# Kernel tuning notes

Measured on AMD Instinct MI355X. Metric: run time of the kernel, lower is better.

Reference implementation:

```python
import jax, jax.numpy as jnp
import numpy as np

CH = 256
IC = 128  # inter_channels = channels // reduction
TEMP = 0.05


def setup_inputs() -> dict:
    key = jax.random.key(0)
    k1, k2, k3, k4, k5 = jax.random.split(key, 5)
    x = jax.random.normal(k1, (8, CH, 64, 64), dtype=jnp.float32)
    # 1x1 conv weights stored as [out_ch, in_ch]
    w_qkv = jax.random.normal(k2, (3 * IC, CH), dtype=jnp.float32) * 0.01
    b_qkv = jax.random.normal(k3, (3 * IC,), dtype=jnp.float32) * 0.01
    w_out = jax.random.normal(k4, (CH, IC), dtype=jnp.float32) * 0.01
    b_out = jax.random.normal(k5, (CH,), dtype=jnp.float32) * 0.01
    return {"x": x, "w_qkv": w_qkv, "b_qkv": b_qkv, "w_out": w_out, "b_out": b_out}


def reference(x, w_qkv, b_qkv, w_out, b_out):
    b, c, h, w = x.shape
    n = h * w
    ic = w_qkv.shape[0] // 3
    # 1x1 conv QKV projection
    qkv = jnp.einsum('bchw,oc->bohw', x, w_qkv) + b_qkv[None, :, None, None]
    qkv = qkv.reshape(b, 3, ic, n)
    q, k, v = qkv[:, 0], qkv[:, 1], qkv[:, 2]  # each [b, ic, n]
    # mean-center q and k over spatial positions (per channel)
    k = k - k.mean(axis=-1, keepdims=True)
    q = q - q.mean(axis=-1, keepdims=True)
    # pairwise_weight[b, i, j] = sum_c k[b, c, i] * q[b, c, j]
    pw = jnp.einsum('bci,bcj->bij', k, q)
    pw = pw / jnp.sqrt(jnp.float32(ic))  # use_scale=True
    pw = pw / TEMP
    pw = jax.nn.softmax(pw, axis=-1)  # [b, n, n]
    # y[b, c, i] = sum_j pw[b, i, j] * v[b, c, j]
    y = jnp.einsum('bij,bcj->bci', pw, v).reshape(b, ic, h, w)
    out = x + jnp.einsum('bchw,oc->bohw', y, w_out) + b_out[None, :, None, None]
    return out
```

## Files before the change

### kernel.cpp

```cpp
#include <hip/hip_runtime.h>
#include <hip/hip_bf16.h>

typedef __bf16 bf16_t;
typedef __bf16 bf16x8 __attribute__((ext_vector_type(8)));
typedef float f32x4 __attribute__((ext_vector_type(4)));
typedef float f32x16 __attribute__((ext_vector_type(16)));

#define MFMA16(a, b, c) __builtin_amdgcn_mfma_f32_16x16x32_bf16((a), (b), (c), 0, 0, 0)
#define MFMA32(a, b, c) __builtin_amdgcn_mfma_f32_32x32x16_bf16((a), (b), (c), 0, 0, 0)

constexpr int CH = 256, IC = 128, NPOS = 4096;
constexpr float SM_C = 2.5503488f;

constexpr size_t OFF_XT    = 0;
constexpr size_t OFF_QT    = 16777216;
constexpr size_t OFF_KT    = 25165824;
constexpr size_t OFF_V     = 33554432;
constexpr size_t OFF_WQKV  = 41943040;
constexpr size_t OFF_WOUT  = 42139648;
constexpr size_t OFF_XMEAN = 42205184;
constexpr size_t OFF_QKM   = 42213376;
constexpr size_t OFF_PL    = 42221568;

__device__ __forceinline__ void gload_lds16(const char* g, char* lds) {
    __builtin_amdgcn_global_load_lds((const __attribute__((address_space(1))) unsigned int*)g,
                                     (__attribute__((address_space(3))) unsigned int*)lds, 16, 0,
                                     0);
}
__device__ __forceinline__ float fexp2(float x) {
    float r;
    asm("v_exp_f32 %0, %1" : "=v"(r) : "v"(x));
    return r;
}
__device__ __forceinline__ int cvtpk(float lo, float hi) {
    int r;
    asm("v_cvt_pk_bf16_f32 %0, %1, %2" : "=v"(r) : "v"(lo), "v"(hi));
    return r;
}

__global__ void k_prep0(const float* __restrict__ wqkv, const float* __restrict__ wout,
                        const float* __restrict__ x, bf16_t* __restrict__ wqkv_b,
                        bf16_t* __restrict__ wout_b, float* __restrict__ xmean) {
    int bid = blockIdx.x;
    if (bid < 512) {
        int idx = bid * 256 + threadIdx.x;
        if (idx < 384 * 256) wqkv_b[idx] = (bf16_t)wqkv[idx];
        int j = idx - 384 * 256;
        if (j >= 0 && j < 256 * 128) wout_b[j] = (bf16_t)wout[j];
        return;
    }
    int xbid = bid - 512;
    int c = xbid & 255, b = xbid >> 8;
    const float4* xv = (const float4*)(x + ((size_t)(b * CH + c)) * NPOS);
    float s = 0.f;
#pragma unroll
    for (int r = 0; r < 4; r++) {
        float4 v = xv[r * 256 + threadIdx.x];
        s += v.x + v.y + v.z + v.w;
    }
    __shared__ float red[256];
    red[threadIdx.x] = s;
    __syncthreads();
    for (int st = 128; st > 0; st >>= 1) {
        if (threadIdx.x < st) red[threadIdx.x] += red[threadIdx.x + st];
        __syncthreads();
    }
    if (threadIdx.x == 0) xmean[b * CH + c] = red[0] * (1.0f / NPOS);
}

__global__ void k_prep1(const float* __restrict__ x, const float* __restrict__ wqkv,
                        const float* __restrict__ xmean, bf16_t* __restrict__ xt,
                        float* __restrict__ qkm) {
    int bid = blockIdx.x;
    if (bid >= 8192) {
        int xbid = bid - 8192;
        int wid = threadIdx.x >> 6, lane = threadIdx.x & 63;
        int o = (xbid & 63) * 4 + wid, b = xbid >> 6;
        float4 w = ((const float4*)(wqkv + (size_t)o * CH))[lane];
        float4 xm = ((const float4*)(xmean + b * CH))[lane];
        float s = w.x * xm.x + w.y * xm.y + w.z * xm.z + w.w * xm.w;
#pragma unroll
        for (int m = 1; m < 64; m <<= 1) s += __shfl_xor(s, m, 64);
        if (lane == 0) qkm[b * CH + o] = s;
        return;
    }
    __shared__ float t[32][33];
    int p0 = (bid & 127) * 32, c0 = ((bid >> 7) & 7) * 32, b = bid >> 10;
    int i = threadIdx.x >> 5, j = threadIdx.x & 31;
#pragma unroll
    for (int q = 0; q < 4; q++) {
        int c = c0 + q * 8 + i;
        t[q * 8 + i][j] = x[((size_t)(b * CH + c)) * NPOS + p0 + j];
    }
    __syncthreads();
#pragma unroll
    for (int q = 0; q < 4; q++) {
        int p = p0 + q * 8 + i;
        xt[((size_t)(b * NPOS + p)) * CH + c0 + j] = (bf16_t)t[j][q * 8 + i];
    }
}

__global__ __launch_bounds__(256, 2) void k_qkv(const bf16_t* __restrict__ xt,
                                                const bf16_t* __restrict__ wqkv_b,
                                                const float* __restrict__ qkm,
                                                const float* __restrict__ b_qkv,
                                                bf16_t* __restrict__ qt, bf16_t* __restrict__ kt,
                                                bf16_t* __restrict__ v) {
    int bid = blockIdx.x;
    int b = bid & 7;
    int r0 = bid >> 3;
    int sec = r0 % 3;
    int pt = r0 / 3;
    int p0 = pt * 128;
    int wid = threadIdx.x >> 6, lane = threadIdx.x & 63;
    int g = lane >> 4, li = lane & 15;
    int wr = wid >> 1, wc = wid & 1;
    f32x4 acc[4][4] = {};
    if (sec < 2) {
        int ob = sec * 128;
#pragma unroll 1
        for (int kk = 0; kk < 8; kk++) {
            bf16x8 af[4], bfg[4];
#pragma unroll
            for (int fa = 0; fa < 4; fa++) {
                int p = p0 + wr * 64 + fa * 16 + li;
                af[fa] = *(const bf16x8*)(xt + ((size_t)(b * NPOS + p)) * CH + kk * 32 + g * 8);
            }
#pragma unroll
            for (int fb = 0; fb < 4; fb++) {
                int o = ob + wc * 64 + fb * 16 + li;
                bfg[fb] = *(const bf16x8*)(wqkv_b + (size_t)o * CH + kk * 32 + g * 8);
            }
#pragma unroll
            for (int fa = 0; fa < 4; fa++)
#pragma unroll
                for (int fb = 0; fb < 4; fb++) acc[fa][fb] = MFMA16(af[fa], bfg[fb], acc[fa][fb]);
        }
        bf16_t* dst = (sec == 0) ? qt : kt;
        float scale = (sec == 1) ? SM_C : 1.0f;
#pragma unroll
        for (int fb = 0; fb < 4; fb++) {
            int ol = wc * 64 + fb * 16 + li;
            float mean = qkm[b * CH + sec * 128 + ol];
#pragma unroll
            for (int fa = 0; fa < 4; fa++)
#pragma unroll
                for (int r = 0; r < 4; r++) {
                    int p = p0 + wr * 64 + fa * 16 + g * 4 + r;
                    dst[((size_t)(b * NPOS + p)) * IC + ol] =
                        (bf16_t)((acc[fa][fb][r] - mean) * scale);
                }
        }
    } else {
#pragma unroll 1
        for (int kk = 0; kk < 8; kk++) {
            bf16x8 af[4], bfg[4];
#pragma unroll
            for (int fa = 0; fa < 4; fa++) {
                int o = 256 + wr * 64 + fa * 16 + li;
                af[fa] = *(const bf16x8*)(wqkv_b + (size_t)o * CH + kk * 32 + g * 8);
            }
#pragma unroll
            for (int fb = 0; fb < 4; fb++) {
                int p = p0 + wc * 64 + fb * 16 + li;
                bfg[fb] = *(const bf16x8*)(xt + ((size_t)(b * NPOS + p)) * CH + kk * 32 + g * 8);
            }
#pragma unroll
            for (int fa = 0; fa < 4; fa++)
#pragma unroll
                for (int fb = 0; fb < 4; fb++) acc[fa][fb] = MFMA16(af[fa], bfg[fb], acc[fa][fb]);
        }
#pragma unroll
        for (int fa = 0; fa < 4; fa++)
#pragma unroll
            for (int r = 0; r < 4; r++) {
                int oe = wr * 64 + fa * 16 + g * 4 + r;
                float bias = b_qkv[256 + oe];
#pragma unroll
                for (int fb = 0; fb < 4; fb++) {
                    int p = p0 + wc * 64 + fb * 16 + li;
                    v[((size_t)(b * IC + oe)) * NPOS + p] = (bf16_t)(acc[fa][fb][r] + bias);
                }
            }
    }
}

constexpr int TJ = 64;

__global__ __launch_bounds__(256, 2) void k_attn(const bf16_t* __restrict__ qt,
                                                 const bf16_t* __restrict__ kt,
                                                 const bf16_t* __restrict__ v,
                                                 bf16_t* __restrict__ pacc,
                                                 float* __restrict__ pl) {
    __shared__ __attribute__((aligned(128))) char smem[2 * 32768];
    const int bid = blockIdx.x;
    const int b = bid & 7;
    const int r0 = bid >> 3;
    const int jh = r0 & 1;
    const int it = r0 >> 1;
    const int jbase = jh * 2048;
    const int wid = threadIdx.x >> 6, lane = threadIdx.x & 63;
    const int col = lane & 31, h = lane >> 5;
    const int iw0 = it * 128 + wid * 32;
    const bf16_t* ktb = kt + (size_t)b * NPOS * IC;
    const bf16_t* qtb = qt + (size_t)b * NPOS * IC;
    const bf16_t* vb = v + (size_t)b * IC * NPOS;

    int qoff_[4], voff_[4];
#pragma unroll
    for (int u = 0; u < 4; u++) {
        int t = wid * 4 + u;
        int qrow = 4 * t + (lane >> 4);
        qoff_[u] = qrow * 256 + (((lane & 15) ^ (qrow & 15)) << 4);
        int crow = 4 * t + (lane >> 4);
        int src = (lane & 15) ^ (crow & 15);
        voff_[u] = (crow + (src >> 3) * 64) * 8192 + (src & 7) * 16;
    }

    auto stage = [&](int dstpar, int sj) {
        const char* qs = (const char*)qtb + (size_t)sj * 256;
        const char* vs = (const char*)vb + (size_t)sj * 2;
        char* qd = smem + dstpar * 32768;
        char* vd = qd + 16384;
#pragma unroll
        for (int u = 0; u < 4; u++) {
            gload_lds16(qs + qoff_[u], qd + (wid * 4 + u) * 1024);
            gload_lds16(vs + voff_[u], vd + (wid * 4 + u) * 1024);
        }
    };

    stage(0, jbase);

    bf16x8 bk[8];
#pragma unroll
    for (int ks = 0; ks < 8; ks++)
        bk[ks] = *(const bf16x8*)(ktb + (size_t)(iw0 + col) * IC + ks * 16 + h * 8);

    f32x16 acc[4] = {};
    float ls[4] = {0.f, 0.f, 0.f, 0.f};

    auto body = [&](int par, int nextj) {
        stage(par ^ 1, nextj);
        asm volatile("s_waitcnt vmcnt(8)" ::: "memory");
        __builtin_amdgcn_s_barrier();
        asm volatile("" ::: "memory");
        const char* qb = smem + par * 32768;
        const char* vbuf = qb + 16384;
#pragma unroll
        for (int jsub = 0; jsub < 2; jsub++) {
            f32x16 s = {};
            __builtin_amdgcn_s_setprio(1);
#pragma unroll
            for (int ks = 0; ks < 8; ks++) {
                bf16x8 aq = *(const bf16x8*)(qb + (jsub * 32 + col) * 256 +
                                             (((ks * 2 + h) ^ (col & 15)) << 4));
                s = MFMA32(aq, bk[ks], s);
            }
            __builtin_amdgcn_s_setprio(0);
            float e[16];
#pragma unroll
            for (int r = 0; r < 16; r++) e[r] = fexp2(s[r]);
#pragma unroll
            for (int r = 0; r < 16; r++) ls[r & 3] += e[r];
            int w[8];
#pragma unroll
            for (int q = 0; q < 8; q++) w[q] = cvtpk(e[2 * q], e[2 * q + 1]);
            asm("v_permlane32_swap_b32 %0, %1" : "+v"(w[0]), "+v"(w[2]));
            asm("v_permlane32_swap_b32 %0, %1" : "+v"(w[1]), "+v"(w[3]));
            asm("v_permlane32_swap_b32 %0, %1" : "+v"(w[4]), "+v"(w[6]));
            asm("v_permlane32_swap_b32 %0, %1" : "+v"(w[5]), "+v"(w[7]));
            union {
                int u[4];
                bf16x8 v;
            } pb0, pb1;
            pb0.u[0] = w[0]; pb0.u[1] = w[1]; pb0.u[2] = w[2]; pb0.u[3] = w[3];
            pb1.u[0] = w[4]; pb1.u[1] = w[5]; pb1.u[2] = w[6]; pb1.u[3] = w[7];
            __builtin_amdgcn_s_setprio(1);
#pragma unroll
            for (int kl = 0; kl < 2; kl++) {
                int kg = jsub * 2 + kl;
                bf16x8 pbf = kl == 0 ? pb0.v : pb1.v;
#pragma unroll
                for (int cs = 0; cs < 4; cs++) {
                    int crow = (cs & 1) * 32 + col;
                    int p = ((cs >> 1) * 8 + kg * 2 + h) ^ (crow & 15);
                    bf16x8 av = *(const bf16x8*)(vbuf + crow * 256 + (p << 4));
                    acc[cs] = MFMA32(av, pbf, acc[cs]);
                }
            }
            __builtin_amdgcn_s_setprio(0);
        }
        asm volatile("" ::: "memory");
        __builtin_amdgcn_s_barrier();
    };

#pragma unroll 1
    for (int jo = 0; jo < 2048; jo += 2 * TJ) {
        body(0, jbase + ((jo + TJ) & 2047));
        body(1, jbase + ((jo + 2 * TJ) & 2047));
    }

    float lsum = (ls[0] + ls[1]) + (ls[2] + ls[3]);
    lsum += __shfl_xor(lsum, 32, 64);
    const int i = iw0 + col;
    if (h == 0) pl[((size_t)(b * 2 + jh)) * NPOS + i] = lsum;

    bf16_t* po = pacc + ((size_t)(b * 2 + jh)) * NPOS * IC;
#pragma unroll
    for (int cs = 0; cs < 4; cs++)
#pragma unroll
        for (int q = 0; q < 8; q++) {
            int u = cvtpk(acc[cs][2 * q], acc[cs][2 * q + 1]);
            int c0 = cs * 32 + ((q & 1) << 1) + ((q >> 1) << 3) + 4 * h;
            *(int*)((char*)po + ((size_t)i * IC + c0) * 2) = u;
        }
}

__global__ __launch_bounds__(256, 2) void k_out(const bf16_t* __restrict__ pacc,
                                                const float* __restrict__ pl,
                                                const bf16_t* __restrict__ wout_b,
                                                const float* __restrict__ x,
                                                const float* __restrict__ b_out,
                                                float* __restrict__ out) {
    int bid = blockIdx.x;
    int b = bid & 7;
    int r0 = bid >> 3;
    int oct = r0 & 1, pt = r0 >> 1;
    int p0 = pt * 128, oc0 = oct * 128;
    int wid = threadIdx.x >> 6, lane = threadIdx.x & 63;
    int g = lane >> 4, li = lane & 15;
    int wr = wid >> 1, wc = wid & 1;
    const bf16_t* pa0 = pacc + (size_t)(b * 2 + 0) * NPOS * IC;
    const bf16_t* pa1 = pacc + (size_t)(b * 2 + 1) * NPOS * IC;
    float inv[4];
#pragma unroll
    for (int fb = 0; fb < 4; fb++) {
        int p = p0 + wc * 64 + fb * 16 + li;
        inv[fb] = 1.0f / (pl[(size_t)(b * 2 + 0) * NPOS + p] + pl[(size_t)(b * 2 + 1) * NPOS + p]);
    }
    f32x4 acc[4][4] = {};
#pragma unroll
    for (int kk = 0; kk < 4; kk++) {
        bf16x8 af[4], bfg[4];
#pragma unroll
        for (int fa = 0; fa < 4; fa++) {
            int oc = oc0 + wr * 64 + fa * 16 + li;
            af[fa] = *(const bf16x8*)(wout_b + (size_t)oc * IC + kk * 32 + g * 8);
        }
#pragma unroll
        for (int fb = 0; fb < 4; fb++) {
            int p = p0 + wc * 64 + fb * 16 + li;
            bf16x8 a0 = *(const bf16x8*)(pa0 + (size_t)p * IC + kk * 32 + g * 8);
            bf16x8 a1 = *(const bf16x8*)(pa1 + (size_t)p * IC + kk * 32 + g * 8);
#pragma unroll
            for (int e = 0; e < 8; e++)
                bfg[fb][e] = (bf16_t)(((float)a0[e] + (float)a1[e]) * inv[fb]);
        }
#pragma unroll
        for (int fa = 0; fa < 4; fa++)
#pragma unroll
            for (int fb = 0; fb < 4; fb++) acc[fa][fb] = MFMA16(af[fa], bfg[fb], acc[fa][fb]);
    }
#pragma unroll
    for (int fa = 0; fa < 4; fa++)
#pragma unroll
        for (int r = 0; r < 4; r++) {
            int oc = oc0 + wr * 64 + fa * 16 + g * 4 + r;
            float bias = b_out[oc];
#pragma unroll
            for (int fb = 0; fb < 4; fb++) {
                int p = p0 + wc * 64 + fb * 16 + li;
                size_t idx = ((size_t)(b * CH + oc)) * NPOS + p;
                out[idx] = acc[fa][fb][r] + x[idx] + bias;
            }
        }
}

extern "C" void kernel_launch(void* const* d_in, const int* in_sizes, int n_in, void* d_out,
                              int out_size, void* d_ws, size_t ws_size, hipStream_t stream) {
    const float* x = (const float*)d_in[0];
    const float* w_qkv = (const float*)d_in[1];
    const float* b_qkv = (const float*)d_in[2];
    const float* w_out = (const float*)d_in[3];
    const float* b_out = (const float*)d_in[4];
    float* out = (float*)d_out;
    char* ws = (char*)d_ws;

    bf16_t* xt = (bf16_t*)(ws + OFF_XT);
    bf16_t* pacc = (bf16_t*)(ws + OFF_XT);
    bf16_t* qt = (bf16_t*)(ws + OFF_QT);
    bf16_t* kt = (bf16_t*)(ws + OFF_KT);
    bf16_t* v = (bf16_t*)(ws + OFF_V);
    bf16_t* wqkv_b = (bf16_t*)(ws + OFF_WQKV);
    bf16_t* wout_b = (bf16_t*)(ws + OFF_WOUT);
    float* xmean = (float*)(ws + OFF_XMEAN);
    float* qkm = (float*)(ws + OFF_QKM);
    float* pl = (float*)(ws + OFF_PL);

    k_prep0<<<2560, 256, 0, stream>>>(w_qkv, w_out, x, wqkv_b, wout_b, xmean);
    k_prep1<<<8704, 256, 0, stream>>>(x, w_qkv, xmean, xt, qkm);
    k_qkv<<<768, 256, 0, stream>>>(xt, wqkv_b, qkm, b_qkv, qt, kt, v);
    k_attn<<<512, 256, 0, stream>>>(qt, kt, v, pacc, pl);
    k_out<<<512, 256, 0, stream>>>(pacc, pl, wout_b, x, b_out, out);
}
```

Before: 142.1 us.

## Split attention key tiles across two warps per row block with LDS reduction

Doubles the attention block to 512 threads. Each pair of warps now covers the same 32 query rows, and each warp of the pair handles one of the two 32-column j-subtiles in every staged tile, instead of one warp walking both subtiles serially. The partial P·V accumulators and softmax row sums are combined through LDS at the end before the bf16 store. This raises wave-level parallelism and MFMA concurrency per CU, at the cost of extra LDS, an end-of-kernel reduction and higher occupancy demands under launch_bounds(512,4).

```diff
diff --git a/kernel.cpp b/kernel.cpp
--- a/kernel.cpp
+++ b/kernel.cpp
@@ -187,34 +187,33 @@
 
 constexpr int TJ = 64;
 
-__global__ __launch_bounds__(256, 2) void k_attn(const bf16_t* __restrict__ qt,
+__global__ __launch_bounds__(512, 4) void k_attn(const bf16_t* __restrict__ qt,
                                                  const bf16_t* __restrict__ kt,
                                                  const bf16_t* __restrict__ v,
                                                  bf16_t* __restrict__ pacc,
                                                  float* __restrict__ pl) {
-    __shared__ __attribute__((aligned(128))) char smem[2 * 32768];
+    __shared__ __attribute__((aligned(128))) char smem[2 * 32768 + 1024];
     const int bid = blockIdx.x;
     const int b = bid & 7;
-    const int r0 = bid >> 3;
-    const int jh = r0 & 1;
-    const int it = r0 >> 1;
+    const int jh = (bid >> 3) & 1;
+    const int it = bid >> 4;
     const int jbase = jh * 2048;
-    const int wid = threadIdx.x >> 6, lane = threadIdx.x & 63;
+    const int t = threadIdx.x;
+    const int wid = t >> 6, lane = t & 63;
     const int col = lane & 31, h = lane >> 5;
-    const int iw0 = it * 128 + wid * 32;
+    const int jw = wid & 1, ih = wid >> 1;
+    const int iw0 = it * 128 + ih * 32;
     const bf16_t* ktb = kt + (size_t)b * NPOS * IC;
     const bf16_t* qtb = qt + (size_t)b * NPOS * IC;
     const bf16_t* vb = v + (size_t)b * IC * NPOS;
 
-    int qoff_[4], voff_[4];
-#pragma unroll
-    for (int u = 0; u < 4; u++) {
-        int t = wid * 4 + u;
-        int qrow = 4 * t + (lane >> 4);
-        qoff_[u] = qrow * 256 + (((lane & 15) ^ (qrow & 15)) << 4);
-        int crow = 4 * t + (lane >> 4);
-        int src = (lane & 15) ^ (crow & 15);
-        voff_[u] = (crow + (src >> 3) * 64) * 8192 + (src & 7) * 16;
+    int qoff_[2], voff_[2];
+#pragma unroll
+    for (int u = 0; u < 2; u++) {
+        int row = u * 32 + (t >> 4);
+        qoff_[u] = row * 256 + (((t & 15) ^ (row & 15)) << 4);
+        int src = (t & 15) ^ (row & 15);
+        voff_[u] = (row + (src >> 3) * 64) * 8192 + (src & 7) * 16;
     }
 
     auto stage = [&](int dstpar, int sj) {
@@ -223,9 +222,9 @@
         char* qd = smem + dstpar * 32768;
         char* vd = qd + 16384;
 #pragma unroll
-        for (int u = 0; u < 4; u++) {
-            gload_lds16(qs + qoff_[u], qd + (wid * 4 + u) * 1024);
-            gload_lds16(vs + voff_[u], vd + (wid * 4 + u) * 1024);
+        for (int u = 0; u < 2; u++) {
+            gload_lds16(qs + qoff_[u], qd + u * 8192 + t * 16);
+            gload_lds16(vs + voff_[u], vd + u * 8192 + t * 16);
         }
     };
 
@@ -241,55 +240,52 @@
 
     auto body = [&](int par, int nextj) {
         stage(par ^ 1, nextj);
-        asm volatile("s_waitcnt vmcnt(8)" ::: "memory");
+        asm volatile("s_waitcnt vmcnt(4)" ::: "memory");
         __builtin_amdgcn_s_barrier();
         asm volatile("" ::: "memory");
         const char* qb = smem + par * 32768;
         const char* vbuf = qb + 16384;
-#pragma unroll
-        for (int jsub = 0; jsub < 2; jsub++) {
-            f32x16 s = {};
-            __builtin_amdgcn_s_setprio(1);
-#pragma unroll
-            for (int ks = 0; ks < 8; ks++) {
-                bf16x8 aq = *(const bf16x8*)(qb + (jsub * 32 + col) * 256 +
-                                             (((ks * 2 + h) ^ (col & 15)) << 4));
-                s = MFMA32(aq, bk[ks], s);
-            }
-            __builtin_amdgcn_s_setprio(0);
-            float e[16];
-#pragma unroll
-            for (int r = 0; r < 16; r++) e[r] = fexp2(s[r]);
-#pragma unroll
-            for (int r = 0; r < 16; r++) ls[r & 3] += e[r];
-            int w[8];
-#pragma unroll
-            for (int q = 0; q < 8; q++) w[q] = cvtpk(e[2 * q], e[2 * q + 1]);
-            asm("v_permlane32_swap_b32 %0, %1" : "+v"(w[0]), "+v"(w[2]));
-            asm("v_permlane32_swap_b32 %0, %1" : "+v"(w[1]), "+v"(w[3]));
-            asm("v_permlane32_swap_b32 %0, %1" : "+v"(w[4]), "+v"(w[6]));
-            asm("v_permlane32_swap_b32 %0, %1" : "+v"(w[5]), "+v"(w[7]));
-            union {
-                int u[4];
-                bf16x8 v;
-            } pb0, pb1;
-            pb0.u[0] = w[0]; pb0.u[1] = w[1]; pb0.u[2] = w[2]; pb0.u[3] = w[3];
-            pb1.u[0] = w[4]; pb1.u[1] = w[5]; pb1.u[2] = w[6]; pb1.u[3] = w[7];
-            __builtin_amdgcn_s_setprio(1);
-#pragma unroll
-            for (int kl = 0; kl < 2; kl++) {
-                int kg = jsub * 2 + kl;
-                bf16x8 pbf = kl == 0 ? pb0.v : pb1.v;
-#pragma unroll
-                for (int cs = 0; cs < 4; cs++) {
-                    int crow = (cs & 1) * 32 + col;
-                    int p = ((cs >> 1) * 8 + kg * 2 + h) ^ (crow & 15);
-                    bf16x8 av = *(const bf16x8*)(vbuf + crow * 256 + (p << 4));
-                    acc[cs] = MFMA32(av, pbf, acc[cs]);
-                }
-            }
-            __builtin_amdgcn_s_setprio(0);
-        }
+        f32x16 s = {};
+        __builtin_amdgcn_s_setprio(1);
+#pragma unroll
+        for (int ks = 0; ks < 8; ks++) {
+            bf16x8 aq = *(const bf16x8*)(qb + (jw * 32 + col) * 256 +
+                                         (((ks * 2 + h) ^ (col & 15)) << 4));
+            s = MFMA32(aq, bk[ks], s);
+        }
+        __builtin_amdgcn_s_setprio(0);
+        float e[16];
+#pragma unroll
+        for (int r = 0; r < 16; r++) e[r] = fexp2(s[r]);
+#pragma unroll
+        for (int r = 0; r < 16; r++) ls[r & 3] += e[r];
+        int w[8];
+#pragma unroll
+        for (int q = 0; q < 8; q++) w[q] = cvtpk(e[2 * q], e[2 * q + 1]);
+        asm("v_permlane32_swap_b32 %0, %1" : "+v"(w[0]), "+v"(w[2]));
+        asm("v_permlane32_swap_b32 %0, %1" : "+v"(w[1]), "+v"(w[3]));
+        asm("v_permlane32_swap_b32 %0, %1" : "+v"(w[4]), "+v"(w[6]));
+        asm("v_permlane32_swap_b32 %0, %1" : "+v"(w[5]), "+v"(w[7]));
+        union {
+            int u[4];
+            bf16x8 v;
+        } pb0, pb1;
+        pb0.u[0] = w[0]; pb0.u[1] = w[1]; pb0.u[2] = w[2]; pb0.u[3] = w[3];
+        pb1.u[0] = w[4]; pb1.u[1] = w[5]; pb1.u[2] = w[6]; pb1.u[3] = w[7];
+        __builtin_amdgcn_s_setprio(1);
+#pragma unroll
+        for (int kl = 0; kl < 2; kl++) {
+            int kg = jw * 2 + kl;
+            bf16x8 pbf = kl == 0 ? pb0.v : pb1.v;
+#pragma unroll
+            for (int cs = 0; cs < 4; cs++) {
+                int crow = (cs & 1) * 32 + col;
+                int p = ((cs >> 1) * 8 + kg * 2 + h) ^ (crow & 15);
+                bf16x8 av = *(const bf16x8*)(vbuf + crow * 256 + (p << 4));
+                acc[cs] = MFMA32(av, pbf, acc[cs]);
+            }
+        }
+        __builtin_amdgcn_s_setprio(0);
         asm volatile("" ::: "memory");
         __builtin_amdgcn_s_barrier();
     };
@@ -300,20 +296,48 @@
         body(1, jbase + ((jo + 2 * TJ) & 2047));
     }
 
+    asm volatile("s_waitcnt vmcnt(0)" ::: "memory");
+    __syncthreads();
+    float* rb = (float*)smem;
+    float* lsb = (float*)(smem + 65536);
     float lsum = (ls[0] + ls[1]) + (ls[2] + ls[3]);
-    lsum += __shfl_xor(lsum, 32, 64);
-    const int i = iw0 + col;
-    if (h == 0) pl[((size_t)(b * 2 + jh)) * NPOS + i] = lsum;
-
-    bf16_t* po = pacc + ((size_t)(b * 2 + jh)) * NPOS * IC;
-#pragma unroll
-    for (int cs = 0; cs < 4; cs++)
-#pragma unroll
-        for (int q = 0; q < 8; q++) {
-            int u = cvtpk(acc[cs][2 * q], acc[cs][2 * q + 1]);
-            int c0 = cs * 32 + ((q & 1) << 1) + ((q >> 1) << 3) + 4 * h;
-            *(int*)((char*)po + ((size_t)i * IC + c0) * 2) = u;
-        }
+    if (jw == 1) {
+        float* db = rb + ih * 4096;
+#pragma unroll
+        for (int cs = 0; cs < 4; cs++)
+#pragma unroll
+            for (int q = 0; q < 4; q++) {
+                f32x4 tv = {acc[cs][4 * q], acc[cs][4 * q + 1], acc[cs][4 * q + 2],
+                            acc[cs][4 * q + 3]};
+                *(f32x4*)(db + (cs * 4 + q) * 256 + lane * 4) = tv;
+            }
+        lsb[ih * 64 + lane] = lsum;
+    }
+    __syncthreads();
+    if (jw == 0) {
+        const float* db = rb + ih * 4096;
+        lsum += lsb[ih * 64 + lane];
+        lsum += __shfl_xor(lsum, 32, 64);
+        const int i = iw0 + col;
+        if (h == 0) pl[((size_t)(b * 2 + jh)) * NPOS + i] = lsum;
+        bf16_t* po = pacc + ((size_t)(b * 2 + jh)) * NPOS * IC;
+#pragma unroll
+        for (int cs = 0; cs < 4; cs++) {
+            f32x16 A = acc[cs];
+#pragma unroll
+            for (int q = 0; q < 4; q++) {
+                f32x4 r = *(const f32x4*)(db + (cs * 4 + q) * 256 + lane * 4);
+#pragma unroll
+                for (int e2 = 0; e2 < 4; e2++) A[4 * q + e2] += r[e2];
+            }
+#pragma unroll
+            for (int q = 0; q < 8; q++) {
+                int u = cvtpk(A[2 * q], A[2 * q + 1]);
+                int c0 = cs * 32 + ((q & 1) << 1) + ((q >> 1) << 3) + 4 * h;
+                *(int*)((char*)po + ((size_t)i * IC + c0) * 2) = u;
+            }
+        }
+    }
 }
 
 __global__ __launch_bounds__(256, 2) void k_out(const bf16_t* __restrict__ pacc,
@@ -400,6 +424,6 @@
     k_prep0<<<2560, 256, 0, stream>>>(w_qkv, w_out, x, wqkv_b, wout_b, xmean);
     k_prep1<<<8704, 256, 0, stream>>>(x, w_qkv, xmean, xt, qkm);
     k_qkv<<<768, 256, 0, stream>>>(xt, wqkv_b, qkm, b_qkv, qt, kt, v);
-    k_attn<<<512, 256, 0, stream>>>(qt, kt, v, pacc, pl);
+    k_attn<<<512, 512, 0, stream>>>(qt, kt, v, pacc, pl);
     k_out<<<512, 256, 0, stream>>>(pacc, pl, wout_b, x, b_out, out);
 }
```

Result: slower. 258.4 us (+81.8%).

## Halve attention j-tile to 32 and raise occupancy to four blocks per CU

Applied to the files above, without the earlier changes.

Shrinks the per-stage key tile in the attention kernel from 64 to 32 positions, halving LDS per block, and raises launch bounds to allow four resident blocks per CU instead of two. The Q and V staging layout and swizzle are rewritten for the smaller tile and the inner loop loses its jsub level. The aim is better latency hiding through more resident waves. The cost is twice as many barriers and pipeline stages per sweep and tighter register limits, which could cause spills.

```diff
diff --git a/kernel.cpp b/kernel.cpp
--- a/kernel.cpp
+++ b/kernel.cpp
@@ -185,47 +185,47 @@
     }
 }
 
-constexpr int TJ = 64;
-
-__global__ __launch_bounds__(256, 2) void k_attn(const bf16_t* __restrict__ qt,
+constexpr int TJ = 32;
+
+__global__ __launch_bounds__(256, 4) void k_attn(const bf16_t* __restrict__ qt,
                                                  const bf16_t* __restrict__ kt,
                                                  const bf16_t* __restrict__ v,
                                                  bf16_t* __restrict__ pacc,
                                                  float* __restrict__ pl) {
-    __shared__ __attribute__((aligned(128))) char smem[2 * 32768];
+    __shared__ __attribute__((aligned(128))) char smem[2 * 16384];
     const int bid = blockIdx.x;
     const int b = bid & 7;
-    const int r0 = bid >> 3;
-    const int jh = r0 & 1;
-    const int it = r0 >> 1;
+    const int jh = (bid >> 3) & 1;
+    const int it = bid >> 4;
     const int jbase = jh * 2048;
-    const int wid = threadIdx.x >> 6, lane = threadIdx.x & 63;
+    const int t = threadIdx.x;
+    const int wid = t >> 6, lane = t & 63;
     const int col = lane & 31, h = lane >> 5;
     const int iw0 = it * 128 + wid * 32;
     const bf16_t* ktb = kt + (size_t)b * NPOS * IC;
     const bf16_t* qtb = qt + (size_t)b * NPOS * IC;
     const bf16_t* vb = v + (size_t)b * IC * NPOS;
 
-    int qoff_[4], voff_[4];
-#pragma unroll
-    for (int u = 0; u < 4; u++) {
-        int t = wid * 4 + u;
-        int qrow = 4 * t + (lane >> 4);
-        qoff_[u] = qrow * 256 + (((lane & 15) ^ (qrow & 15)) << 4);
-        int crow = 4 * t + (lane >> 4);
-        int src = (lane & 15) ^ (crow & 15);
-        voff_[u] = (crow + (src >> 3) * 64) * 8192 + (src & 7) * 16;
+    int qoff_[2], voff_[2];
+#pragma unroll
+    for (int u = 0; u < 2; u++) {
+        int li2 = u * 256 + t;
+        int row = li2 >> 4, p = li2 & 15;
+        qoff_[u] = row * 256 + ((p ^ (row & 15)) << 4);
+        int g = p ^ (row & 15);
+        int c = (g >> 2) * 32 + row;
+        voff_[u] = c * 8192 + (g & 3) * 16;
     }
 
     auto stage = [&](int dstpar, int sj) {
         const char* qs = (const char*)qtb + (size_t)sj * 256;
         const char* vs = (const char*)vb + (size_t)sj * 2;
-        char* qd = smem + dstpar * 32768;
-        char* vd = qd + 16384;
-#pragma unroll
-        for (int u = 0; u < 4; u++) {
-            gload_lds16(qs + qoff_[u], qd + (wid * 4 + u) * 1024);
-            gload_lds16(vs + voff_[u], vd + (wid * 4 + u) * 1024);
+        char* qd = smem + dstpar * 16384;
+        char* vd = qd + 8192;
+#pragma unroll
+        for (int u = 0; u < 2; u++) {
+            gload_lds16(qs + qoff_[u], qd + (u * 256 + t) * 16);
+            gload_lds16(vs + voff_[u], vd + (u * 256 + t) * 16);
         }
     };
 
@@ -241,55 +241,49 @@
 
     auto body = [&](int par, int nextj) {
         stage(par ^ 1, nextj);
-        asm volatile("s_waitcnt vmcnt(8)" ::: "memory");
+        asm volatile("s_waitcnt vmcnt(4)" ::: "memory");
         __builtin_amdgcn_s_barrier();
         asm volatile("" ::: "memory");
-        const char* qb = smem + par * 32768;
-        const char* vbuf = qb + 16384;
-#pragma unroll
-        for (int jsub = 0; jsub < 2; jsub++) {
-            f32x16 s = {};
-            __builtin_amdgcn_s_setprio(1);
-#pragma unroll
-            for (int ks = 0; ks < 8; ks++) {
-                bf16x8 aq = *(const bf16x8*)(qb + (jsub * 32 + col) * 256 +
-                                             (((ks * 2 + h) ^ (col & 15)) << 4));
-                s = MFMA32(aq, bk[ks], s);
-            }
-            __builtin_amdgcn_s_setprio(0);
-            float e[16];
-#pragma unroll
-            for (int r = 0; r < 16; r++) e[r] = fexp2(s[r]);
-#pragma unroll
-            for (int r = 0; r < 16; r++) ls[r & 3] += e[r];
-            int w[8];
-#pragma unroll
-            for (int q = 0; q < 8; q++) w[q] = cvtpk(e[2 * q], e[2 * q + 1]);
-            asm("v_permlane32_swap_b32 %0, %1" : "+v"(w[0]), "+v"(w[2]));
-            asm("v_permlane32_swap_b32 %0, %1" : "+v"(w[1]), "+v"(w[3]));
-            asm("v_permlane32_swap_b32 %0, %1" : "+v"(w[4]), "+v"(w[6]));
-            asm("v_permlane32_swap_b32 %0, %1" : "+v"(w[5]), "+v"(w[7]));
-            union {
-                int u[4];
-                bf16x8 v;
-            } pb0, pb1;
-            pb0.u[0] = w[0]; pb0.u[1] = w[1]; pb0.u[2] = w[2]; pb0.u[3] = w[3];
-            pb1.u[0] = w[4]; pb1.u[1] = w[5]; pb1.u[2] = w[6]; pb1.u[3] = w[7];
-            __builtin_amdgcn_s_setprio(1);
-#pragma unroll
-            for (int kl = 0; kl < 2; kl++) {
-                int kg = jsub * 2 + kl;
-                bf16x8 pbf = kl == 0 ? pb0.v : pb1.v;
-#pragma unroll
-                for (int cs = 0; cs < 4; cs++) {
-                    int crow = (cs & 1) * 32 + col;
-                    int p = ((cs >> 1) * 8 + kg * 2 + h) ^ (crow & 15);
-                    bf16x8 av = *(const bf16x8*)(vbuf + crow * 256 + (p << 4));
-                    acc[cs] = MFMA32(av, pbf, acc[cs]);
-                }
-            }
-            __builtin_amdgcn_s_setprio(0);
-        }
+        const char* qb = smem + par * 16384;
+        const char* vbuf = qb + 8192;
+        f32x16 s = {};
+        __builtin_amdgcn_s_setprio(1);
+#pragma unroll
+        for (int ks = 0; ks < 8; ks++) {
+            bf16x8 aq = *(const bf16x8*)(qb + col * 256 + (((ks * 2 + h) ^ (col & 15)) << 4));
+            s = MFMA32(aq, bk[ks], s);
+        }
+        __builtin_amdgcn_s_setprio(0);
+        float e[16];
+#pragma unroll
+        for (int r = 0; r < 16; r++) e[r] = fexp2(s[r]);
+#pragma unroll
+        for (int r = 0; r < 16; r++) ls[r & 3] += e[r];
+        int w[8];
+#pragma unroll
+        for (int q = 0; q < 8; q++) w[q] = cvtpk(e[2 * q], e[2 * q + 1]);
+        asm("v_permlane32_swap_b32 %0, %1" : "+v"(w[0]), "+v"(w[2]));
+        asm("v_permlane32_swap_b32 %0, %1" : "+v"(w[1]), "+v"(w[3]));
+        asm("v_permlane32_swap_b32 %0, %1" : "+v"(w[4]), "+v"(w[6]));
+        asm("v_permlane32_swap_b32 %0, %1" : "+v"(w[5]), "+v"(w[7]));
+        union {
+            int u[4];
+            bf16x8 v;
+        } pb0, pb1;
+        pb0.u[0] = w[0]; pb0.u[1] = w[1]; pb0.u[2] = w[2]; pb0.u[3] = w[3];
+        pb1.u[0] = w[4]; pb1.u[1] = w[5]; pb1.u[2] = w[6]; pb1.u[3] = w[7];
+        __builtin_amdgcn_s_setprio(1);
+#pragma unroll
+        for (int kg = 0; kg < 2; kg++) {
+            bf16x8 pbf = kg == 0 ? pb0.v : pb1.v;
+#pragma unroll
+            for (int cs = 0; cs < 4; cs++) {
+                bf16x8 av = *(const bf16x8*)(vbuf + col * 256 +
+                                             (((cs * 4 + kg * 2 + h) ^ (col & 15)) << 4));
+                acc[cs] = MFMA32(av, pbf, acc[cs]);
+            }
+        }
+        __builtin_amdgcn_s_setprio(0);
         asm volatile("" ::: "memory");
         __builtin_amdgcn_s_barrier();
     };
```

After: 232.8 us. +63.8%, slower.
